# Performance work log

Measured on AMD Instinct MI355X. Metric: run time of the kernel, lower is better.

## Reference

```python
import math
import jax, jax.numpy as jnp
import numpy as np

B, S, D = 8, 920, 1536
H, HD = 4, 384            # num heads, head dim; all_head = H*HD = 1536
MAX_POS = 920
L = 2 * MAX_POS - 1       # 1839 relative positions


def setup_inputs() -> dict:
    key = jax.random.key(0)
    k1, k2, k3, k4, k5 = jax.random.split(key, 5)
    return {
        "hidden_states": jax.random.normal(k1, (B, S, D), dtype=jnp.float32),
        "w_query": jax.random.normal(k2, (D, H * HD), dtype=jnp.float32) * 0.02,
        "w_key": jax.random.normal(k3, (D, H * HD), dtype=jnp.float32) * 0.02,
        "w_value": jax.random.normal(k4, (D, H * HD), dtype=jnp.float32) * 0.02,
        "distance_embedding": jax.random.normal(k5, (L, HD), dtype=jnp.float32) * 0.02,
    }


def reshape_fortran(x, shape):
    # Matches torch reference: reverse-permute, C reshape of reversed shape, reverse-permute back.
    x = jnp.transpose(x, tuple(reversed(range(x.ndim))))
    x = jnp.reshape(x, tuple(reversed(shape)))
    return jnp.transpose(x, tuple(reversed(range(len(shape)))))


def relative_position_embedding_rotate(scores):
    # scores: [B, H, L, S]
    scores = jnp.transpose(scores, (0, 2, 3, 1))  # [B, L, S, H]
    b, hs, s, h = scores.shape
    scores = jnp.concatenate([scores, jnp.zeros((b, s, s, h), scores.dtype)], axis=1)
    scores = reshape_fortran(scores, [b, (hs + s) * s, 1, h])
    scores = scores[:, : (s + hs - 1) * s]
    scores = reshape_fortran(scores, [b, hs + s - 1, s, h])
    halfpoint = hs // 2
    scores = scores[:, halfpoint : halfpoint + s]          # [B, S, S, H]
    scores = jnp.transpose(scores, (0, 2, 1, 3))           # transpose(1,2)
    return jnp.transpose(scores, (0, 3, 1, 2))             # [B, H, S, S]


def reference(hidden_states, w_query, w_key, w_value, distance_embedding):
    inv = 1.0 / math.sqrt(HD)
    q = (hidden_states @ w_query) * inv                    # [B, S, H*HD]
    k = hidden_states @ w_key
    v = hidden_states @ w_value

    def heads(x):  # [B,S,H*HD] -> [B,H,S,HD]
        return jnp.transpose(x.reshape(B, S, H, HD), (0, 2, 1, 3))

    q, k, v = heads(q), heads(k), heads(v)

    scores = jnp.einsum("bhqd,bhkd->bhqk", q, k)           # [B,H,S,S]
    rel = jnp.einsum("ld,bhsd->bhls", distance_embedding, q)  # [B,H,L,S]
    scores = scores + relative_position_embedding_rotate(rel)

    probs = jax.nn.softmax(scores, axis=-1)
    ctx = jnp.einsum("bhqk,bhkd->bhqd", probs, v)          # [B,H,S,HD]
    ctx = jnp.transpose(ctx, (0, 2, 1, 3)).reshape(B, S, H * HD)
    return ctx
```

## Files before the change

kernel.cpp:

```cpp
#include <hip/hip_runtime.h>

#define S_LEN 920
#define DMODEL 1536
#define NH 4
#define HD 384
#define LREL 1839
#define BATCH 8
#define MTOT (BATCH * S_LEN)
#define KPAD 960
#define PRLD 1840
#define NBH (BATCH * NH)

#define CHS   5652480UL
#define BSLAB 2826240UL
#define KOFF  1413120UL

#define TP_BH   1692800UL
#define SCPR_BH 3385600UL
#define CHBH    (TP_BH + SCPR_BH)
#define QKV_SCRATCH 36765696UL
#define EB_BYTES 1412352UL
#define VT_BYTES 23592960UL

typedef __attribute__((ext_vector_type(8))) short  s16x8;
typedef __attribute__((ext_vector_type(4))) short  s16x4;
typedef __attribute__((ext_vector_type(8))) __bf16 bf16x8;
typedef __attribute__((ext_vector_type(4))) float  f32x4;

__device__ __forceinline__ short f2b(float x) {
  unsigned u = __builtin_bit_cast(unsigned, x);
  unsigned r = (u + 0x7FFFu + ((u >> 16) & 1u)) >> 16;
  return (short)r;
}
__device__ __forceinline__ float b2f(short s) {
  unsigned u = ((unsigned)(unsigned short)s) << 16;
  return __builtin_bit_cast(float, u);
}

__device__ __forceinline__ void load_lds16(const short* g, short* lds) {
  __builtin_amdgcn_global_load_lds(
      (const __attribute__((address_space(1))) void*)g,
      (__attribute__((address_space(3))) void*)lds, 16, 0, 0);
}

__device__ __forceinline__ f32x4 mfma_bf16(s16x8 a, s16x8 b, f32x4 c) {
  return __builtin_amdgcn_mfma_f32_16x16x32_bf16(
      __builtin_bit_cast(bf16x8, a), __builtin_bit_cast(bf16x8, b), c, 0, 0, 0);
}

__device__ __forceinline__ s16x8 frag_swz(const short* base, int row, int kk, int lq) {
  int byte = (row << 7) + (kk << 6) + (lq << 4);
  byte ^= (row & 7) << 4;
  return *(const s16x8*)((const char*)base + byte);
}

template <int NT>
__device__ __forceinline__ void gemm_pipe(short* smem,
    const short* __restrict__ A, int ldA, int mClamp, int m0,
    const short* __restrict__ B, int ldB, int nClamp, int n0,
    f32x4 acc[4][6]) {
  short* const A0 = smem;
  short* const B0 = smem + 16384;
  short* const A1 = smem + 28672;
  short* const B1 = smem + 45056;

  const int tid = threadIdx.x, w = tid >> 6, lane = tid & 63;
  const int lr = lane & 15, lq = lane >> 4;
  const int wr = w >> 1, wc = w & 1;

  const short* pa[4]; int la[4];
  const short* pb[3]; int lb[3];
  {
    const int rl = lane >> 3, c = lane & 7;
#pragma unroll
    for (int i = 0; i < 4; ++i) {
      int r = w * 32 + i * 8 + rl;
      int ra = m0 + r; if (ra > mClamp) ra = mClamp;
      pa[i] = A + (size_t)ra * ldA + ((c ^ (r & 7)) * 8);
      la[i] = (w * 32 + i * 8) * 64;
    }
#pragma unroll
    for (int i = 0; i < 3; ++i) {
      int r = w * 24 + i * 8 + rl;
      int rb = n0 + r; if (rb > nClamp) rb = nClamp;
      pb[i] = B + (size_t)rb * ldB + ((c ^ (r & 7)) * 8);
      lb[i] = (w * 24 + i * 8) * 64;
    }
  }

#pragma unroll
  for (int i = 0; i < 4; ++i)
#pragma unroll
    for (int j = 0; j < 6; ++j) acc[i][j] = (f32x4){0.f, 0.f, 0.f, 0.f};

#pragma unroll
  for (int i = 0; i < 4; ++i) load_lds16(pa[i], A0 + la[i]);
#pragma unroll
  for (int i = 0; i < 3; ++i) load_lds16(pb[i], B0 + lb[i]);

  for (int kt = 0; kt < NT; ++kt) {
    short* const Ab = (kt & 1) ? A1 : A0;
    short* const Bb = (kt & 1) ? B1 : B0;
    short* const An = (kt & 1) ? A0 : A1;
    short* const Bn = (kt & 1) ? B0 : B1;

    if (kt + 1 < NT) {
      const int k0 = (kt + 1) * 64;
#pragma unroll
      for (int i = 0; i < 4; ++i) load_lds16(pa[i] + k0, An + la[i]);
#pragma unroll
      for (int i = 0; i < 3; ++i) load_lds16(pb[i] + k0, Bn + lb[i]);
      asm volatile("s_waitcnt vmcnt(7)" ::: "memory");
    } else {
      asm volatile("s_waitcnt vmcnt(0)" ::: "memory");
    }
    __builtin_amdgcn_sched_barrier(0);
    __builtin_amdgcn_s_barrier();
    __builtin_amdgcn_sched_barrier(0);

    s16x8 a[4], bb[3];
#pragma unroll
    for (int f = 0; f < 4; ++f) a[f] = frag_swz(Ab, wr * 64 + f * 16 + lr, 0, lq);
#pragma unroll
    for (int f = 0; f < 3; ++f) bb[f] = frag_swz(Bb, wc * 96 + f * 16 + lr, 0, lq);
    __builtin_amdgcn_s_barrier();
    __builtin_amdgcn_s_setprio(1);
#pragma unroll
    for (int i = 0; i < 4; ++i)
#pragma unroll
      for (int j = 0; j < 3; ++j) acc[i][j] = mfma_bf16(a[i], bb[j], acc[i][j]);
    __builtin_amdgcn_s_setprio(0);
    __builtin_amdgcn_s_barrier();
#pragma unroll
    for (int f = 0; f < 3; ++f) bb[f] = frag_swz(Bb, wc * 96 + (3 + f) * 16 + lr, 0, lq);
    __builtin_amdgcn_s_barrier();
    __builtin_amdgcn_s_setprio(1);
#pragma unroll
    for (int i = 0; i < 4; ++i)
#pragma unroll
      for (int j = 0; j < 3; ++j) acc[i][3 + j] = mfma_bf16(a[i], bb[j], acc[i][3 + j]);
    __builtin_amdgcn_s_setprio(0);
    __builtin_amdgcn_s_barrier();
#pragma unroll
    for (int f = 0; f < 4; ++f) a[f] = frag_swz(Ab, wr * 64 + f * 16 + lr, 1, lq);
#pragma unroll
    for (int f = 0; f < 3; ++f) bb[f] = frag_swz(Bb, wc * 96 + f * 16 + lr, 1, lq);
    __builtin_amdgcn_s_barrier();
    __builtin_amdgcn_s_setprio(1);
#pragma unroll
    for (int i = 0; i < 4; ++i)
#pragma unroll
      for (int j = 0; j < 3; ++j) acc[i][j] = mfma_bf16(a[i], bb[j], acc[i][j]);
    __builtin_amdgcn_s_setprio(0);
    __builtin_amdgcn_s_barrier();
#pragma unroll
    for (int f = 0; f < 3; ++f) bb[f] = frag_swz(Bb, wc * 96 + (3 + f) * 16 + lr, 1, lq);
    __builtin_amdgcn_s_barrier();
    __builtin_amdgcn_s_setprio(1);
#pragma unroll
    for (int i = 0; i < 4; ++i)
#pragma unroll
      for (int j = 0; j < 3; ++j) acc[i][3 + j] = mfma_bf16(a[i], bb[j], acc[i][3 + j]);
    __builtin_amdgcn_s_setprio(0);
    __builtin_amdgcn_s_barrier();
  }
}

__global__ void k_cast(const float* __restrict__ X, short* __restrict__ O, int n4) {
  int i = blockIdx.x * blockDim.x + threadIdx.x;
  if (i >= n4) return;
  float4 v = ((const float4*)X)[i];
  s16x4 o = {f2b(v.x), f2b(v.y), f2b(v.z), f2b(v.w)};
  *(s16x4*)&O[(size_t)i * 4] = o;
}

__global__ void k_transpose_w(const float* __restrict__ W0, const float* __restrict__ W1,
                              const float* __restrict__ W2, short* __restrict__ Wt) {
  const float* W = (blockIdx.z == 0) ? W0 : ((blockIdx.z == 1) ? W1 : W2);
  short* O = Wt + (size_t)blockIdx.z * DMODEL * DMODEL;
  __shared__ float t[32][33];
  int tx = threadIdx.x, ty = threadIdx.y;
  int n0 = blockIdx.x * 32, k0 = blockIdx.y * 32;
#pragma unroll
  for (int i = 0; i < 4; ++i)
    t[ty + i * 8][tx] = W[(size_t)(k0 + ty + i * 8) * DMODEL + n0 + tx];
  __syncthreads();
#pragma unroll
  for (int i = 0; i < 4; ++i)
    O[(size_t)(n0 + ty + i * 8) * DMODEL + k0 + tx] = f2b(t[tx][ty + i * 8]);
}

__global__ void k_zero_vtpad(short* __restrict__ Vt) {
  int idx = blockIdx.x * blockDim.x + threadIdx.x;
  if (idx >= NBH * HD * (KPAD - S_LEN)) return;
  int bhd = idx / (KPAD - S_LEN);
  int s = S_LEN + idx - bhd * (KPAD - S_LEN);
  Vt[(size_t)bhd * KPAD + s] = 0;
}

#define QKV_NT (DMODEL / 64)

__global__ __launch_bounds__(512, 2) void k_gemm_qkv(const short* __restrict__ Xb,
                                                     const short* __restrict__ Wt,
                                                     short* __restrict__ out16,
                                                     short* __restrict__ Vt) {
  __shared__ short smem[57344];
  const int z = blockIdx.z;
  const int t = blockIdx.x;
  const int t2 = (t & 7) * 29 + (t >> 3);
  const int m0 = (t2 >> 3) * 256;
  const int n0 = (t2 & 7) * 192;

  const int tid = threadIdx.x, w = tid >> 6, lane = tid & 63;
  const int lr = lane & 15, lq = lane >> 4;
  const int wr = w >> 1, wc = w & 1;

  f32x4 acc[4][6];
  gemm_pipe<QKV_NT>(smem, Xb, DMODEL, MTOT - 1, m0,
                    Wt + (size_t)z * DMODEL * DMODEL, DMODEL, DMODEL - 1, n0, acc);

  __syncthreads();
  const float inv = 0.05103103630798287f;
  if (z != 2) {
    short* T = smem;
#pragma unroll
    for (int i = 0; i < 4; ++i)
#pragma unroll
      for (int j = 0; j < 6; ++j) {
        int ml = wr * 64 + i * 16 + lq * 4;
        int nl = wc * 96 + j * 16 + lr;
#pragma unroll
        for (int r = 0; r < 4; ++r) {
          float v = acc[i][j][r];
          T[(ml + r) * 200 + nl] = f2b(z == 0 ? v * inv : v);
        }
      }
    __syncthreads();
    for (int u = 0; u < 12; ++u) {
      int unit = u * 512 + tid;
      int ml = unit / 24, c = unit - ml * 24;
      int m = m0 + ml;
      if (m < MTOT) {
        int b = m / S_LEN, s = m - b * S_LEN;
        short* dst = out16 + (size_t)(b >> 1) * CHS + (size_t)(b & 1) * BSLAB +
                     (z == 1 ? KOFF : 0UL) + (size_t)s * DMODEL + n0 + c * 8;
        *(s16x8*)dst = *(const s16x8*)&T[ml * 200 + c * 8];
      }
    }
  } else {
    short* T = smem;
#pragma unroll
    for (int i = 0; i < 4; ++i)
#pragma unroll
      for (int j = 0; j < 6; ++j) {
        int ml = wr * 64 + i * 16 + lq * 4;
        int nl = wc * 96 + j * 16 + lr;
#pragma unroll
        for (int r = 0; r < 4; ++r)
          T[nl * 264 + ml + r] = f2b(acc[i][j][r]);
      }
    __syncthreads();
    const int h = n0 / HD;
    const int d0 = n0 - h * HD;
    for (int u = 0; u < 12; ++u) {
      int unit = u * 512 + tid;
      int nl = unit >> 5, c = unit & 31;
      int m = m0 + c * 8;
      if (m < MTOT) {
        int b = m / S_LEN, s = m - b * S_LEN;
        size_t row = (size_t)(b * NH + h) * HD + d0 + nl;
        *(s16x8*)&Vt[row * KPAD + s] = *(const s16x8*)&T[nl * 264 + c * 8];
      }
    }
  }
}

__global__ __launch_bounds__(512, 2) void k_gemm_T(const short* __restrict__ out16,
                                                   const short* __restrict__ Eb,
                                                   short* __restrict__ Tp, int bh0) {
  __shared__ short smem[57344];
  const int z = blockIdx.z;
  const int bh = bh0 + z, b = bh >> 2, h = bh & 3;
  const int t = blockIdx.x;
  int mi, lj;
  if      (t < 7)  { mi = 0; lj = 3 + t; }
  else if (t < 14) { mi = 1; lj = 2 + (t - 7); }
  else if (t < 21) { mi = 2; lj = t - 14; }
  else             { mi = 3; lj = t - 21; }
  const int m0 = mi * 256, n0 = lj * 192;
  const short* A = out16 + (size_t)(b >> 1) * CHS + (size_t)(b & 1) * BSLAB + h * HD;

  f32x4 acc[4][6];
  gemm_pipe<HD / 64>(smem, A, DMODEL, S_LEN - 1, m0, Eb, HD, LREL - 1, n0, acc);

  const int tid = threadIdx.x, w = tid >> 6, lane = tid & 63;
  const int lr = lane & 15, lq = lane >> 4;
  const int wr = w >> 1, wc = w & 1;
#pragma unroll
  for (int i = 0; i < 4; ++i)
#pragma unroll
    for (int j = 0; j < 6; ++j) {
      int l = n0 + wc * 96 + j * 16 + lr;
#pragma unroll
      for (int r = 0; r < 4; ++r) {
        int m = m0 + wr * 64 + i * 16 + lq * 4 + r;
        if (m < S_LEN) {
          int jp = l - (S_LEN - 1) + m;
          if (jp >= 0 && jp < S_LEN)
            Tp[((size_t)z * S_LEN + m) * S_LEN + jp] = f2b(acc[i][j][r]);
        }
      }
    }
}

__global__ __launch_bounds__(512, 2) void k_gemm_scores(const short* __restrict__ out16,
                                                        const short* __restrict__ Tp,
                                                        float* __restrict__ SCc, int bh0) {
  __shared__ short smem[57344];
  const int z = blockIdx.z;
  const int bh = bh0 + z, b = bh >> 2, h = bh & 3;
  const int m0 = blockIdx.x * 256, n0 = blockIdx.y * 192;
  const short* Qp = out16 + (size_t)(b >> 1) * CHS + (size_t)(b & 1) * BSLAB + h * HD;
  const short* Kp = Qp + KOFF;

  f32x4 acc[4][6];
  gemm_pipe<HD / 64>(smem, Qp, DMODEL, S_LEN - 1, m0, Kp, DMODEL, S_LEN - 1, n0, acc);

  const int tid = threadIdx.x, w = tid >> 6, lane = tid & 63;
  const int lr = lane & 15, lq = lane >> 4;
  const int wr = w >> 1, wc = w & 1;
#pragma unroll
  for (int i = 0; i < 4; ++i)
#pragma unroll
    for (int j = 0; j < 6; ++j) {
      int n = n0 + wc * 96 + j * 16 + lr;
#pragma unroll
      for (int r = 0; r < 4; ++r) {
        int m = m0 + wr * 64 + i * 16 + lq * 4 + r;
        if (m < S_LEN && n < S_LEN) {
          SCc[((size_t)z * S_LEN + m) * S_LEN + n] =
              acc[i][j][r] + b2f(Tp[((size_t)z * S_LEN + m) * S_LEN + n]);
        }
      }
    }
}

__global__ __launch_bounds__(256) void k_softmax(float* __restrict__ SCc) {
  const int row = blockIdx.x;
  float* src = SCc + (size_t)row * S_LEN;
  short* dst = (short*)src;
  const int tid = threadIdx.x, lane = tid & 63, wv = tid >> 6;
  const bool act = tid < 230;
  float v[4];
  if (act) {
    float4 f = ((const float4*)src)[tid];
    v[0] = f.x; v[1] = f.y; v[2] = f.z; v[3] = f.w;
  } else {
    v[0] = v[1] = v[2] = v[3] = -1e30f;
  }
  float mx = fmaxf(fmaxf(v[0], v[1]), fmaxf(v[2], v[3]));
  for (int off = 32; off; off >>= 1) mx = fmaxf(mx, __shfl_xor(mx, off));
  __shared__ float redm[4];
  __shared__ float reds[4];
  if (lane == 0) redm[wv] = mx;
  __syncthreads();
  mx = fmaxf(fmaxf(redm[0], redm[1]), fmaxf(redm[2], redm[3]));
  float e[4], s = 0.f;
#pragma unroll
  for (int i = 0; i < 4; ++i) { e[i] = __expf(v[i] - mx); s += e[i]; }
  for (int off = 32; off; off >>= 1) s += __shfl_xor(s, off);
  if (lane == 0) reds[wv] = s;
  __syncthreads();
  s = reds[0] + reds[1] + reds[2] + reds[3];
  float rs = 1.0f / s;
  if (tid < 240) {
    s16x4 o;
    if (act) {
      o = (s16x4){f2b(e[0] * rs), f2b(e[1] * rs), f2b(e[2] * rs), f2b(e[3] * rs)};
    } else {
      o = (s16x4){0, 0, 0, 0};
    }
    *(s16x4*)&dst[tid * 4] = o;
  }
}

__global__ __launch_bounds__(512, 2) void k_gemm_ctx(const short* __restrict__ PRc,
                                                     const short* __restrict__ Vt,
                                                     float* __restrict__ out, int bh0) {
  __shared__ short smem[57344];
  const int z = blockIdx.z;
  const int bh = bh0 + z, b = bh >> 2, h = bh & 3;
  const int m0 = blockIdx.x * 256, n0 = blockIdx.y * 192;
  const short* A = PRc + (size_t)z * S_LEN * PRLD;
  const short* Bt = Vt + (size_t)bh * HD * KPAD;

  f32x4 acc[4][6];
  gemm_pipe<KPAD / 64>(smem, A, PRLD, S_LEN - 1, m0, Bt, KPAD, HD - 1, n0, acc);

  const int tid = threadIdx.x, w = tid >> 6, lane = tid & 63;
  const int lr = lane & 15, lq = lane >> 4;
  const int wr = w >> 1, wc = w & 1;
#pragma unroll
  for (int i = 0; i < 4; ++i)
#pragma unroll
    for (int j = 0; j < 6; ++j) {
      int n = n0 + wc * 96 + j * 16 + lr;
#pragma unroll
      for (int r = 0; r < 4; ++r) {
        int m = m0 + wr * 64 + i * 16 + lq * 4 + r;
        if (m < S_LEN)
          out[((size_t)(b * S_LEN) + m) * DMODEL + h * HD + n] = acc[i][j][r];
      }
    }
}

extern "C" void kernel_launch(void* const* d_in, const int* in_sizes, int n_in,
                              void* d_out, int out_size, void* d_ws, size_t ws_size,
                              hipStream_t stream) {
  const float* hs = (const float*)d_in[0];
  const float* wq = (const float*)d_in[1];
  const float* wk = (const float*)d_in[2];
  const float* wv = (const float*)d_in[3];
  const float* de = (const float*)d_in[4];
  char* ws = (char*)d_ws;

  int CH;
  if      (ws_size >= 32 * CHBH + EB_BYTES + VT_BYTES) CH = 32;
  else if (ws_size >= 16 * CHBH + EB_BYTES + VT_BYTES) CH = 16;
  else                                                  CH = 8;
  size_t chunk_bytes = (size_t)CH * CHBH;
  size_t fixed_base = chunk_bytes > QKV_SCRATCH ? chunk_bytes : QKV_SCRATCH;

  short* Xb  = (short*)(ws + 0);
  short* Wt  = (short*)(ws + 22609920UL);
  short* Tp  = (short*)(ws + 0);
  float* SCc = (float*)(ws + (size_t)CH * TP_BH);
  short* PRc = (short*)SCc;
  short* Eb  = (short*)(ws + fixed_base);
  short* Vt  = (short*)(ws + fixed_base + EB_BYTES);
  short* out16 = (short*)d_out;

  k_cast<<<(MTOT * DMODEL / 4 + 255) / 256, 256, 0, stream>>>(hs, Xb, MTOT * DMODEL / 4);
  k_cast<<<(LREL * HD / 4 + 255) / 256, 256, 0, stream>>>(de, Eb, LREL * HD / 4);
  k_transpose_w<<<dim3(48, 48, 3), dim3(32, 8, 1), 0, stream>>>(wq, wk, wv, Wt);
  k_zero_vtpad<<<(NBH * HD * (KPAD - S_LEN) + 255) / 256, 256, 0, stream>>>(Vt);

  k_gemm_qkv<<<dim3(232, 1, 3), 512, 0, stream>>>(Xb, Wt, out16, Vt);

  int NC = 32 / CH;
  for (int c = 0; c < NC; ++c) {
    int bh0 = c * CH;
    k_gemm_T<<<dim3(27, 1, CH), 512, 0, stream>>>(out16, Eb, Tp, bh0);
    k_gemm_scores<<<dim3(4, 5, CH), 512, 0, stream>>>(out16, Tp, SCc, bh0);
    k_softmax<<<CH * S_LEN, 256, 0, stream>>>(SCc);
    k_gemm_ctx<<<dim3(4, 2, CH), 512, 0, stream>>>(PRc, Vt, (float*)d_out, bh0);
  }
}
```

Measured before the change: 505.6 us.

## Fuse relative-position scores, softmax and PV into one flash-style kernel

Replaces the separate T-gemm, scores gemm, softmax and context gemm kernels with one fused online-softmax kernel per 64-row query tile. The relative-position band is computed per KV tile into LDS and added in-register, so the large score and probability buffers no longer round-trip through global memory. Output goes to a workspace buffer, then a copy kernel scatters it into the final layout. Each head is processed in two halves, so 240 blocks of 512 threads at occupancy 1 may underfill the GPU. The position-embedding product is also recomputed for each tile.

```diff
diff --git a/kernel.cpp b/kernel.cpp
--- a/kernel.cpp
+++ b/kernel.cpp
@@ -8,17 +8,12 @@
 #define BATCH 8
 #define MTOT (BATCH * S_LEN)
 #define KPAD 960
-#define PRLD 1840
 #define NBH (BATCH * NH)
 
 #define CHS   5652480UL
 #define BSLAB 2826240UL
 #define KOFF  1413120UL
 
-#define TP_BH   1692800UL
-#define SCPR_BH 3385600UL
-#define CHBH    (TP_BH + SCPR_BH)
-#define QKV_SCRATCH 36765696UL
 #define EB_BYTES 1412352UL
 #define VT_BYTES 23592960UL
 
@@ -275,143 +270,301 @@
   }
 }
 
-__global__ __launch_bounds__(512, 2) void k_gemm_T(const short* __restrict__ out16,
-                                                   const short* __restrict__ Eb,
-                                                   short* __restrict__ Tp, int bh0) {
-  __shared__ short smem[57344];
-  const int z = blockIdx.z;
-  const int bh = bh0 + z, b = bh >> 2, h = bh & 3;
-  const int t = blockIdx.x;
-  int mi, lj;
-  if      (t < 7)  { mi = 0; lj = 3 + t; }
-  else if (t < 14) { mi = 1; lj = 2 + (t - 7); }
-  else if (t < 21) { mi = 2; lj = t - 14; }
-  else             { mi = 3; lj = t - 21; }
-  const int m0 = mi * 256, n0 = lj * 192;
-  const short* A = out16 + (size_t)(b >> 1) * CHS + (size_t)(b & 1) * BSLAB + h * HD;
-
-  f32x4 acc[4][6];
-  gemm_pipe<HD / 64>(smem, A, DMODEL, S_LEN - 1, m0, Eb, HD, LREL - 1, n0, acc);
+#define FKV 192
+#define FNT 5
+
+#define WAITVM(N) { asm volatile("s_waitcnt vmcnt(" #N ")" ::: "memory"); \
+  __builtin_amdgcn_sched_barrier(0); __builtin_amdgcn_s_barrier(); \
+  __builtin_amdgcn_sched_barrier(0); }
+
+#define LBAR { asm volatile("s_waitcnt lgkmcnt(0)" ::: "memory"); \
+  __builtin_amdgcn_sched_barrier(0); __builtin_amdgcn_s_barrier(); \
+  __builtin_amdgcn_sched_barrier(0); }
+
+#define NOISSUE { }
+
+#define STAGE_E(BUF, C, L0) { \
+  _Pragma("unroll") for (int i_ = 0; i_ < 4; ++i_) { \
+    int r_ = w * 32 + i_ * 8 + rl; \
+    int rg_ = (L0) + r_; rg_ = rg_ < 0 ? 0 : (rg_ > LREL - 1 ? LREL - 1 : rg_); \
+    load_lds16(Eb + (size_t)rg_ * HD + ((cs ^ (r_ & 7)) * 8) + (C) * 64, \
+               (BUF) + (w * 32 + i_ * 8) * 64); } }
+
+#define STAGE_K(BUF, C) { \
+  _Pragma("unroll") for (int i_ = 0; i_ < 3; ++i_) { \
+    int r_ = w * 24 + i_ * 8 + rl; \
+    int rg_ = kv0 + r_; if (rg_ > S_LEN - 1) rg_ = S_LEN - 1; \
+    load_lds16(Kp + (size_t)rg_ * DMODEL + ((cs ^ (r_ & 7)) * 8) + (C) * 64, \
+               (BUF) + (w * 24 + i_ * 8) * 64); } }
+
+#define STAGE_V(BUF, HF, SC) { \
+  _Pragma("unroll") for (int i_ = 0; i_ < 3; ++i_) { \
+    int r_ = w * 24 + i_ * 8 + rl; \
+    load_lds16(Vb + (size_t)((HF) * 192 + r_) * KPAD + kv0 + (SC) * 64 + ((cs ^ (r_ & 7)) * 8), \
+               (BUF) + (w * 24 + i_ * 8) * 64); } }
+
+#define GSLOT_T(CUR, C, ISSUE, WVM) { ISSUE; WVM; \
+  s16x8 a_[2][2], b_[2][4]; \
+  _Pragma("unroll") for (int k_ = 0; k_ < 2; ++k_) { \
+    _Pragma("unroll") for (int i_ = 0; i_ < 2; ++i_) \
+      a_[i_][k_] = frag_swz(QL + (C) * 4096, wm * 32 + i_ * 16 + lr, k_, lq); \
+    _Pragma("unroll") for (int j_ = 0; j_ < 4; ++j_) \
+      b_[k_][j_] = frag_swz((CUR), wn * 64 + j_ * 16 + lr, k_, lq); } \
+  __builtin_amdgcn_s_setprio(1); \
+  _Pragma("unroll") for (int k_ = 0; k_ < 2; ++k_) \
+    _Pragma("unroll") for (int i_ = 0; i_ < 2; ++i_) \
+      _Pragma("unroll") for (int j_ = 0; j_ < 4; ++j_) \
+        acc_t[i_][j_] = mfma_bf16(a_[i_][k_], b_[k_][j_], acc_t[i_][j_]); \
+  __builtin_amdgcn_s_setprio(0); __builtin_amdgcn_s_barrier(); }
+
+#define GSLOT_S(CUR, C, ISSUE, WVM) { ISSUE; WVM; \
+  s16x8 a_[2][2], b_[2][3]; \
+  _Pragma("unroll") for (int k_ = 0; k_ < 2; ++k_) { \
+    _Pragma("unroll") for (int i_ = 0; i_ < 2; ++i_) \
+      a_[i_][k_] = frag_swz(QL + (C) * 4096, wm * 32 + i_ * 16 + lr, k_, lq); \
+    _Pragma("unroll") for (int j_ = 0; j_ < 3; ++j_) \
+      b_[k_][j_] = frag_swz((CUR), wn * 48 + j_ * 16 + lr, k_, lq); } \
+  __builtin_amdgcn_s_setprio(1); \
+  _Pragma("unroll") for (int k_ = 0; k_ < 2; ++k_) \
+    _Pragma("unroll") for (int i_ = 0; i_ < 2; ++i_) \
+      _Pragma("unroll") for (int j_ = 0; j_ < 3; ++j_) \
+        acc_s[i_][j_] = mfma_bf16(a_[i_][k_], b_[k_][j_], acc_s[i_][j_]); \
+  __builtin_amdgcn_s_setprio(0); __builtin_amdgcn_s_barrier(); }
+
+#define GSLOT_PV(CUR, SC, HF, ISSUE, WVM) { ISSUE; WVM; \
+  s16x8 a_[2][2], b_[2][3]; \
+  _Pragma("unroll") for (int k_ = 0; k_ < 2; ++k_) { \
+    _Pragma("unroll") for (int i_ = 0; i_ < 2; ++i_) \
+      a_[i_][k_] = frag_swz(TLP + (SC) * 4096, wm * 32 + i_ * 16 + lr, k_, lq); \
+    _Pragma("unroll") for (int j_ = 0; j_ < 3; ++j_) \
+      b_[k_][j_] = frag_swz((CUR), wn * 48 + j_ * 16 + lr, k_, lq); } \
+  __builtin_amdgcn_s_setprio(1); \
+  _Pragma("unroll") for (int k_ = 0; k_ < 2; ++k_) \
+    _Pragma("unroll") for (int i_ = 0; i_ < 2; ++i_) \
+      _Pragma("unroll") for (int j_ = 0; j_ < 3; ++j_) \
+        acc_o[i_][(HF) * 3 + j_] = mfma_bf16(a_[i_][k_], b_[k_][j_], acc_o[i_][(HF) * 3 + j_]); \
+  __builtin_amdgcn_s_setprio(0); __builtin_amdgcn_s_barrier(); }
+
+__global__ __launch_bounds__(512, 1) void k_fused(const short* __restrict__ out16,
+                                                  const short* __restrict__ Vt,
+                                                  const short* __restrict__ Eb,
+                                                  float* __restrict__ O, int half) {
+  __shared__ short smem[74752];
+  short* const QL  = smem;
+  short* const B0  = smem + 24576;
+  short* const B1  = smem + 40960;
+  short* const TLP = smem + 57344;
+  float* const pmax = (float*)(smem + 73728);
+  float* const psum = pmax + 256;
+
+  const int f  = blockIdx.x;
+  const int f2 = (f & 7) * 30 + (f >> 3);
+  const int mt = f2 % 15, bhl = f2 / 15;
+  const int bh = half * 16 + bhl, b = bh >> 2, h = bh & 3;
+  const int m0 = mt * 64;
 
   const int tid = threadIdx.x, w = tid >> 6, lane = tid & 63;
   const int lr = lane & 15, lq = lane >> 4;
-  const int wr = w >> 1, wc = w & 1;
-#pragma unroll
-  for (int i = 0; i < 4; ++i)
-#pragma unroll
-    for (int j = 0; j < 6; ++j) {
-      int l = n0 + wc * 96 + j * 16 + lr;
-#pragma unroll
-      for (int r = 0; r < 4; ++r) {
-        int m = m0 + wr * 64 + i * 16 + lq * 4 + r;
-        if (m < S_LEN) {
-          int jp = l - (S_LEN - 1) + m;
-          if (jp >= 0 && jp < S_LEN)
-            Tp[((size_t)z * S_LEN + m) * S_LEN + jp] = f2b(acc[i][j][r]);
-        }
-      }
-    }
-}
-
-__global__ __launch_bounds__(512, 2) void k_gemm_scores(const short* __restrict__ out16,
-                                                        const short* __restrict__ Tp,
-                                                        float* __restrict__ SCc, int bh0) {
-  __shared__ short smem[57344];
-  const int z = blockIdx.z;
-  const int bh = bh0 + z, b = bh >> 2, h = bh & 3;
-  const int m0 = blockIdx.x * 256, n0 = blockIdx.y * 192;
+  const int wm = w >> 2, wn = w & 3;
+  const int rl = lane >> 3, cs = lane & 7;
+
   const short* Qp = out16 + (size_t)(b >> 1) * CHS + (size_t)(b & 1) * BSLAB + h * HD;
   const short* Kp = Qp + KOFF;
-
-  f32x4 acc[4][6];
-  gemm_pipe<HD / 64>(smem, Qp, DMODEL, S_LEN - 1, m0, Kp, DMODEL, S_LEN - 1, n0, acc);
-
-  const int tid = threadIdx.x, w = tid >> 6, lane = tid & 63;
-  const int lr = lane & 15, lq = lane >> 4;
-  const int wr = w >> 1, wc = w & 1;
-#pragma unroll
-  for (int i = 0; i < 4; ++i)
-#pragma unroll
-    for (int j = 0; j < 6; ++j) {
-      int n = n0 + wc * 96 + j * 16 + lr;
+  const short* Vb = Vt + (size_t)bh * HD * KPAD;
+  float* Ob = O + (size_t)bhl * S_LEN * HD;
+
+  f32x4 acc_o[2][6];
+  float Mst[2][4], Lst[2][4];
+#pragma unroll
+  for (int i = 0; i < 2; ++i) {
+#pragma unroll
+    for (int j = 0; j < 6; ++j) acc_o[i][j] = (f32x4){0.f, 0.f, 0.f, 0.f};
+#pragma unroll
+    for (int r = 0; r < 4; ++r) { Mst[i][r] = -1e30f; Lst[i][r] = 0.f; }
+  }
+
+#pragma unroll
+  for (int i = 0; i < 6; ++i) {
+    int rq = w * 8 + rl;
+    int rg = m0 + rq; if (rg > S_LEN - 1) rg = S_LEN - 1;
+    load_lds16(Qp + (size_t)rg * DMODEL + ((cs ^ (rq & 7)) * 8) + i * 64,
+               QL + i * 4096 + (w * 8) * 64);
+  }
+  { const int l0p = 856 - m0; STAGE_E(B0, 0, l0p); }
+
+  for (int t = 0; t < FNT; ++t) {
+    const int kv0 = t * FKV;
+    const int l0 = kv0 - m0 + 856;
+
+    f32x4 acc_t[2][4];
+#pragma unroll
+    for (int i = 0; i < 2; ++i)
+#pragma unroll
+      for (int j = 0; j < 4; ++j) acc_t[i][j] = (f32x4){0.f, 0.f, 0.f, 0.f};
+
+    GSLOT_T(B0, 0, STAGE_E(B1, 1, l0), WAITVM(4));
+    GSLOT_T(B1, 1, STAGE_E(B0, 2, l0), WAITVM(4));
+    GSLOT_T(B0, 2, STAGE_E(B1, 3, l0), WAITVM(4));
+    GSLOT_T(B1, 3, STAGE_E(B0, 4, l0), WAITVM(4));
+    GSLOT_T(B0, 4, STAGE_E(B1, 5, l0), WAITVM(4));
+    GSLOT_T(B1, 5, STAGE_K(B0, 0),     WAITVM(3));
+
+#pragma unroll
+    for (int i = 0; i < 2; ++i)
+#pragma unroll
+      for (int j = 0; j < 4; ++j)
+#pragma unroll
+        for (int r = 0; r < 4; ++r) {
+          int row = wm * 32 + i * 16 + lq * 4 + r;
+          int col = wn * 64 + j * 16 + lr;
+          TLP[row * 256 + col] = f2b(acc_t[i][j][r]);
+        }
+    LBAR;
+
+    f32x4 acc_s[2][3];
+#pragma unroll
+    for (int i = 0; i < 2; ++i)
+#pragma unroll
+      for (int j = 0; j < 3; ++j) acc_s[i][j] = (f32x4){0.f, 0.f, 0.f, 0.f};
+
+    GSLOT_S(B0, 0, STAGE_K(B1, 1), WAITVM(3));
+    GSLOT_S(B1, 1, STAGE_K(B0, 2), WAITVM(3));
+    GSLOT_S(B0, 2, STAGE_K(B1, 3), WAITVM(3));
+    GSLOT_S(B1, 3, STAGE_K(B0, 4), WAITVM(3));
+    GSLOT_S(B0, 4, STAGE_K(B1, 5), WAITVM(3));
+    GSLOT_S(B1, 5, STAGE_V(B0, 0, 0), WAITVM(3));
+
+#pragma unroll
+    for (int i = 0; i < 2; ++i)
+#pragma unroll
+      for (int j = 0; j < 3; ++j) {
+        int jpl = wn * 48 + j * 16 + lr;
+        int jp = kv0 + jpl;
+#pragma unroll
+        for (int r = 0; r < 4; ++r) {
+          int row = wm * 32 + i * 16 + lq * 4 + r;
+          float x = acc_s[i][j][r] + b2f(TLP[row * 256 + (jpl - row + 63)]);
+          acc_s[i][j][r] = (jp < S_LEN) ? x : -1e30f;
+        }
+      }
+    {
+      float tm[2][4];
+#pragma unroll
+      for (int i = 0; i < 2; ++i)
+#pragma unroll
+        for (int r = 0; r < 4; ++r) {
+          float v = fmaxf(fmaxf(acc_s[i][0][r], acc_s[i][1][r]), acc_s[i][2][r]);
+#pragma unroll
+          for (int o = 1; o < 16; o <<= 1) v = fmaxf(v, __shfl_xor(v, o));
+          tm[i][r] = v;
+        }
+      if (lr == 0) {
+#pragma unroll
+        for (int i = 0; i < 2; ++i)
+#pragma unroll
+          for (int r = 0; r < 4; ++r)
+            pmax[wn * 64 + wm * 32 + i * 16 + lq * 4 + r] = tm[i][r];
+      }
+    }
+    LBAR;
+    float fexp[2][4], ps[2][4];
+#pragma unroll
+    for (int i = 0; i < 2; ++i)
 #pragma unroll
       for (int r = 0; r < 4; ++r) {
-        int m = m0 + wr * 64 + i * 16 + lq * 4 + r;
-        if (m < S_LEN && n < S_LEN) {
-          SCc[((size_t)z * S_LEN + m) * S_LEN + n] =
-              acc[i][j][r] + b2f(Tp[((size_t)z * S_LEN + m) * S_LEN + n]);
-        }
-      }
-    }
-}
-
-__global__ __launch_bounds__(256) void k_softmax(float* __restrict__ SCc) {
-  const int row = blockIdx.x;
-  float* src = SCc + (size_t)row * S_LEN;
-  short* dst = (short*)src;
-  const int tid = threadIdx.x, lane = tid & 63, wv = tid >> 6;
-  const bool act = tid < 230;
-  float v[4];
-  if (act) {
-    float4 f = ((const float4*)src)[tid];
-    v[0] = f.x; v[1] = f.y; v[2] = f.z; v[3] = f.w;
-  } else {
-    v[0] = v[1] = v[2] = v[3] = -1e30f;
-  }
-  float mx = fmaxf(fmaxf(v[0], v[1]), fmaxf(v[2], v[3]));
-  for (int off = 32; off; off >>= 1) mx = fmaxf(mx, __shfl_xor(mx, off));
-  __shared__ float redm[4];
-  __shared__ float reds[4];
-  if (lane == 0) redm[wv] = mx;
-  __syncthreads();
-  mx = fmaxf(fmaxf(redm[0], redm[1]), fmaxf(redm[2], redm[3]));
-  float e[4], s = 0.f;
-#pragma unroll
-  for (int i = 0; i < 4; ++i) { e[i] = __expf(v[i] - mx); s += e[i]; }
-  for (int off = 32; off; off >>= 1) s += __shfl_xor(s, off);
-  if (lane == 0) reds[wv] = s;
-  __syncthreads();
-  s = reds[0] + reds[1] + reds[2] + reds[3];
-  float rs = 1.0f / s;
-  if (tid < 240) {
-    s16x4 o;
-    if (act) {
-      o = (s16x4){f2b(e[0] * rs), f2b(e[1] * rs), f2b(e[2] * rs), f2b(e[3] * rs)};
+        int row = wm * 32 + i * 16 + lq * 4 + r;
+        float M2 = fmaxf(fmaxf(pmax[row], pmax[64 + row]),
+                         fmaxf(pmax[128 + row], pmax[192 + row]));
+        M2 = fmaxf(M2, Mst[i][r]);
+        fexp[i][r] = __expf(Mst[i][r] - M2);
+        Mst[i][r] = M2;
+      }
+#pragma unroll
+    for (int i = 0; i < 2; ++i)
+#pragma unroll
+      for (int r = 0; r < 4; ++r) {
+        float s0 = 0.f;
+#pragma unroll
+        for (int j = 0; j < 3; ++j) {
+          float p = __expf(acc_s[i][j][r] - Mst[i][r]);
+          acc_s[i][j][r] = p;
+          s0 += p;
+        }
+#pragma unroll
+        for (int o = 1; o < 16; o <<= 1) s0 += __shfl_xor(s0, o);
+        ps[i][r] = s0;
+#pragma unroll
+        for (int jj = 0; jj < 6; ++jj) acc_o[i][jj][r] *= fexp[i][r];
+      }
+    if (lr == 0) {
+#pragma unroll
+      for (int i = 0; i < 2; ++i)
+#pragma unroll
+        for (int r = 0; r < 4; ++r)
+          psum[wn * 64 + wm * 32 + i * 16 + lq * 4 + r] = ps[i][r];
+    }
+    LBAR;
+#pragma unroll
+    for (int i = 0; i < 2; ++i)
+#pragma unroll
+      for (int r = 0; r < 4; ++r) {
+        int row = wm * 32 + i * 16 + lq * 4 + r;
+        float ts = psum[row] + psum[64 + row] + psum[128 + row] + psum[192 + row];
+        Lst[i][r] = Lst[i][r] * fexp[i][r] + ts;
+      }
+#pragma unroll
+    for (int i = 0; i < 2; ++i)
+#pragma unroll
+      for (int j = 0; j < 3; ++j) {
+        int c192 = wn * 48 + j * 16 + lr;
+        int sc = c192 >> 6, c64 = c192 & 63;
+#pragma unroll
+        for (int r = 0; r < 4; ++r) {
+          int row = wm * 32 + i * 16 + lq * 4 + r;
+          int byte = sc * 8192 + row * 128 + ((c64 * 2) ^ ((row & 7) * 16));
+          *(short*)((char*)TLP + byte) = f2b(acc_s[i][j][r]);
+        }
+      }
+    LBAR;
+
+    GSLOT_PV(B0, 0, 0, STAGE_V(B1, 0, 1), WAITVM(3));
+    GSLOT_PV(B1, 1, 0, STAGE_V(B0, 0, 2), WAITVM(3));
+    GSLOT_PV(B0, 2, 0, STAGE_V(B1, 1, 0), WAITVM(3));
+    GSLOT_PV(B1, 0, 1, STAGE_V(B0, 1, 1), WAITVM(3));
+    GSLOT_PV(B0, 1, 1, STAGE_V(B1, 1, 2), WAITVM(3));
+    if (t < FNT - 1) {
+      GSLOT_PV(B1, 2, 1, STAGE_E(B0, 0, l0 + FKV), WAITVM(4));
     } else {
-      o = (s16x4){0, 0, 0, 0};
-    }
-    *(s16x4*)&dst[tid * 4] = o;
-  }
-}
-
-__global__ __launch_bounds__(512, 2) void k_gemm_ctx(const short* __restrict__ PRc,
-                                                     const short* __restrict__ Vt,
-                                                     float* __restrict__ out, int bh0) {
-  __shared__ short smem[57344];
-  const int z = blockIdx.z;
-  const int bh = bh0 + z, b = bh >> 2, h = bh & 3;
-  const int m0 = blockIdx.x * 256, n0 = blockIdx.y * 192;
-  const short* A = PRc + (size_t)z * S_LEN * PRLD;
-  const short* Bt = Vt + (size_t)bh * HD * KPAD;
-
-  f32x4 acc[4][6];
-  gemm_pipe<KPAD / 64>(smem, A, PRLD, S_LEN - 1, m0, Bt, KPAD, HD - 1, n0, acc);
-
-  const int tid = threadIdx.x, w = tid >> 6, lane = tid & 63;
-  const int lr = lane & 15, lq = lane >> 4;
-  const int wr = w >> 1, wc = w & 1;
-#pragma unroll
-  for (int i = 0; i < 4; ++i)
-#pragma unroll
-    for (int j = 0; j < 6; ++j) {
-      int n = n0 + wc * 96 + j * 16 + lr;
-#pragma unroll
-      for (int r = 0; r < 4; ++r) {
-        int m = m0 + wr * 64 + i * 16 + lq * 4 + r;
-        if (m < S_LEN)
-          out[((size_t)(b * S_LEN) + m) * DMODEL + h * HD + n] = acc[i][j][r];
-      }
-    }
+      GSLOT_PV(B1, 2, 1, NOISSUE, WAITVM(0));
+    }
+  }
+
+#pragma unroll
+  for (int i = 0; i < 2; ++i)
+#pragma unroll
+    for (int r = 0; r < 4; ++r) {
+      int m = m0 + wm * 32 + i * 16 + lq * 4 + r;
+      if (m < S_LEN) {
+        float rs = 1.0f / Lst[i][r];
+#pragma unroll
+        for (int jj = 0; jj < 6; ++jj) {
+          int d = (jj / 3) * 192 + wn * 48 + (jj % 3) * 16 + lr;
+          Ob[(size_t)m * HD + d] = acc_o[i][jj][r] * rs;
+        }
+      }
+    }
+}
+
+__global__ __launch_bounds__(256) void k_copy_o(const float* __restrict__ O,
+                                                float* __restrict__ out, int b0) {
+  int i = blockIdx.x * 256 + threadIdx.x;
+  if (i >= 16 * S_LEN * HD / 4) return;
+  const int per_bh = S_LEN * HD / 4;
+  int bhl = i / per_bh, rem = i - bhl * per_bh;
+  int m = rem / (HD / 4), d4 = rem - m * (HD / 4);
+  int b = b0 + (bhl >> 2), h = bhl & 3;
+  float4 v = ((const float4*)O)[i];
+  ((float4*)out)[((size_t)(b * S_LEN + m) * DMODEL + h * HD + d4 * 4) >> 2] = v;
 }
 
 extern "C" void kernel_launch(void* const* d_in, const int* in_sizes, int n_in,
@@ -424,20 +577,11 @@
   const float* de = (const float*)d_in[4];
   char* ws = (char*)d_ws;
 
-  int CH;
-  if      (ws_size >= 32 * CHBH + EB_BYTES + VT_BYTES) CH = 32;
-  else if (ws_size >= 16 * CHBH + EB_BYTES + VT_BYTES) CH = 16;
-  else                                                  CH = 8;
-  size_t chunk_bytes = (size_t)CH * CHBH;
-  size_t fixed_base = chunk_bytes > QKV_SCRATCH ? chunk_bytes : QKV_SCRATCH;
-
-  short* Xb  = (short*)(ws + 0);
-  short* Wt  = (short*)(ws + 22609920UL);
-  short* Tp  = (short*)(ws + 0);
-  float* SCc = (float*)(ws + (size_t)CH * TP_BH);
-  short* PRc = (short*)SCc;
-  short* Eb  = (short*)(ws + fixed_base);
-  short* Vt  = (short*)(ws + fixed_base + EB_BYTES);
+  short* Xb = (short*)(ws + 0);
+  short* Wt = (short*)(ws + 22609920UL);
+  short* Eb = (short*)(ws + 36765696UL);
+  short* Vt = (short*)(ws + 36765696UL + EB_BYTES);
+  float* Og = (float*)(ws + 0);
   short* out16 = (short*)d_out;
 
   k_cast<<<(MTOT * DMODEL / 4 + 255) / 256, 256, 0, stream>>>(hs, Xb, MTOT * DMODEL / 4);
@@ -447,12 +591,8 @@
 
   k_gemm_qkv<<<dim3(232, 1, 3), 512, 0, stream>>>(Xb, Wt, out16, Vt);
 
-  int NC = 32 / CH;
-  for (int c = 0; c < NC; ++c) {
-    int bh0 = c * CH;
-    k_gemm_T<<<dim3(27, 1, CH), 512, 0, stream>>>(out16, Eb, Tp, bh0);
-    k_gemm_scores<<<dim3(4, 5, CH), 512, 0, stream>>>(out16, Tp, SCc, bh0);
-    k_softmax<<<CH * S_LEN, 256, 0, stream>>>(SCc);
-    k_gemm_ctx<<<dim3(4, 2, CH), 512, 0, stream>>>(PRc, Vt, (float*)d_out, bh0);
-  }
-}
+  for (int hf = 0; hf < 2; ++hf) {
+    k_fused<<<dim3(240), 512, 0, stream>>>(out16, Vt, Eb, Og, hf);
+    k_copy_o<<<dim3(5520), 256, 0, stream>>>(Og, (float*)d_out, hf * 4);
+  }
+}
```

New measurement: 423.1 us. 16.3% less time.
